# Performance work log

Measured on AMD Instinct MI355X. Metric: run time of the kernel, lower is better.

Reference implementation:

```python
import jax, jax.numpy as jnp
import numpy as np

H, D, VD = 8, 64, 64
QD, KD, VDIM, OUT = 512, 512, 512, 512
N, QS, VS = 16, 512, 512
TEMP = 10.0              # softstair_temp
SCALING = D ** -0.5


def _softstair(x):
    fl = jnp.floor(x)
    return fl + jax.nn.sigmoid(TEMP * (jnp.abs(x - fl) - 0.5))


def setup_inputs() -> dict:
    key = jax.random.key(0)
    ks = jax.random.split(key, 24)
    f = jax.random.normal
    s = 0.03  # xavier-ish scale
    return {
        "Q": f(ks[0], (N, QS, QD), jnp.float32),
        "K": f(ks[1], (N, VS, KD), jnp.float32),
        "V": f(ks[2], (N, VS, VDIM), jnp.float32),
        "past_state": f(ks[3], (N, H, QS, D), jnp.float32),
        "past_attention": jax.random.uniform(ks[4], (N, H, QS, 1), jnp.float32),
        "value_positions": jnp.arange(VS, dtype=jnp.float32),
        "attention_mask": jnp.ones((N, QS, VS), jnp.int32),
        "Wq": f(ks[5], (QD, H * D), jnp.float32) * s,
        "Wk": f(ks[6], (KD, H * D), jnp.float32) * s,
        "Wv": f(ks[7], (VDIM, H * VD), jnp.float32) * s,
        "Wpos": f(ks[8], (QD, H * D), jnp.float32) * s,
        "bpos": f(ks[9], (H * D,), jnp.float32) * s,
        "Wsigma": f(ks[10], (H, D, 1), jnp.float32) * s,
        "Wrho": f(ks[11], (H, D, 3), jnp.float32) * s,
        "mix_w": f(ks[12], (QD, 1), jnp.float32) * s,
        "mix_b": f(ks[13], (1,), jnp.float32) * s,
        "gru_wi": f(ks[14], (D, 3 * D), jnp.float32) * s,
        "gru_wh": f(ks[15], (D, 3 * D), jnp.float32) * s,
        "gru_bi": f(ks[16], (3 * D,), jnp.float32) * s,
        "gru_bh": f(ks[17], (3 * D,), jnp.float32) * s,
        "Wc": f(ks[18], (H * VD, OUT), jnp.float32) * s,
    }


def reference(Q, K, V, past_state, past_attention, value_positions, attention_mask,
              Wq, Wk, Wv, Wpos, bpos, Wsigma, Wrho, mix_w, mix_b,
              gru_wi, gru_wh, gru_bi, gru_bh, Wc):
    n, qS, _ = Q.shape
    vS = K.shape[1]
    mask_f = attention_mask.astype(jnp.float32)          # [N,qS,vS]
    mask_b = attention_mask.astype(bool)[:, None]        # [N,1,qS,vS]
    lengths = jnp.sum(mask_f, axis=-1)                   # [N,qS]
    l_1 = jnp.maximum(1.0, lengths - 1.0)[:, None, :, None]
    step_size = 1.0 / l_1                                # [N,1,qS,1]
    nvp = value_positions[None, None, None, :] * step_size  # [N,1,qS,vS]

    # mix gate
    mix = jax.nn.sigmoid(Q @ mix_w + mix_b)[:, None]     # [N,1,qS,1]

    # projections -> [N,H,S,d]
    Qpos = (Q @ Wpos + bpos).reshape(n, qS, H, D).transpose(0, 2, 1, 3)
    Qh = (Q @ Wq).reshape(n, qS, H, D).transpose(0, 2, 1, 3)
    Kh = (K @ Wk).reshape(n, vS, H, D).transpose(0, 2, 1, 3)
    Vh = (V @ Wv).reshape(n, vS, H, VD).transpose(0, 2, 1, 3)

    # content attention
    content = jnp.einsum('bhqd,bhkd->bhqk', Qh, Kh) * SCALING
    content_attn = jax.nn.softmax(jnp.where(mask_b, content, -jnp.inf), axis=-1)

    # GRUCell update (torch gate order r,z,n) on relu(Qpos) with past_state
    x = jax.nn.relu(Qpos)
    gi = x @ gru_wi + gru_bi
    gh = past_state @ gru_wh + gru_bh
    ir, iz, inn = jnp.split(gi, 3, axis=-1)
    hr, hz, hn = jnp.split(gh, 3, axis=-1)
    r = jax.nn.sigmoid(ir + hr)
    z = jax.nn.sigmoid(iz + hz)
    nn_ = jnp.tanh(inn + r * hn)
    state = (1.0 - z) * nn_ + z * past_state             # [N,H,qS,D]

    # location (Gaussian) attention
    sigma = (jax.nn.relu(jnp.einsum('bhqd,hde->bhqe', state, Wsigma)) + 0.27) \
            / lengths[:, None, :, None]                  # [N,H,qS,1]
    rho = jnp.einsum('bhqd,hde->bhqe', state, Wrho)      # [N,H,qS,3]
    steps = _softstair(rho[..., 0:1])
    attn_gate = jax.nn.sigmoid(rho[..., 1:2])
    bias_gate = jax.nn.sigmoid(rho[..., 2:3])
    mu_ = steps * step_size + attn_gate * past_attention + bias_gate
    # leaky clamp to [0,1]
    mu = jnp.maximum(0.01 * mu_, jnp.minimum(mu_, 1.0 + 0.01 * mu_))
    diff = nvp - mu                                      # [N,H,qS,vS]
    gauss = jnp.exp(-(diff * diff) / (2.0 * sigma * sigma))
    g = gauss * mask_f[:, None]
    pos_attn = g / jnp.sum(g + 1e-20, axis=-1, keepdims=True)

    scores = mix * pos_attn + (1.0 - mix) * content_attn
    attended = jnp.einsum('bhqk,bhkv->bhqv', scores, Vh)
    out = attended.transpose(0, 2, 1, 3).reshape(n, qS, H * VD) @ Wc
    return out
```

## Files before the change

### kernel.cpp

```cpp
#include <hip/hip_runtime.h>


typedef __bf16 bf16;
typedef __bf16 bfx8 __attribute__((ext_vector_type(8)));
typedef float v4f __attribute__((ext_vector_type(4)));

__device__ inline float sigm(float x) { return 1.0f / (1.0f + __expf(-x)); }
__device__ inline float tanh_fast(float x) { return 1.0f - 2.0f / (__expf(2.0f * x) + 1.0f); }

__device__ inline v4f mfma16(bfx8 a, bfx8 b, v4f c) {
    return __builtin_amdgcn_mfma_f32_16x16x32_bf16(a, b, c, 0, 0, 0);
}

__device__ inline void split8(const float* __restrict__ p, bfx8& hi, bfx8& lo) {
    float4 x = *(const float4*)p;
    float4 y = *(const float4*)(p + 4);
    float v[8] = {x.x, x.y, x.z, x.w, y.x, y.y, y.z, y.w};
#pragma unroll
    for (int j = 0; j < 8; ++j) {
        bf16 h = (bf16)v[j];
        hi[j] = h;
        lo[j] = (bf16)(v[j] - (float)h);
    }
}

__device__ inline bfx8 cvt8(const float* __restrict__ p) {
    float4 x = *(const float4*)p;
    float4 y = *(const float4*)(p + 4);
    bfx8 o;
    o[0] = (bf16)x.x; o[1] = (bf16)x.y; o[2] = (bf16)x.z; o[3] = (bf16)x.w;
    o[4] = (bf16)y.x; o[5] = (bf16)y.y; o[6] = (bf16)y.z; o[7] = (bf16)y.w;
    return o;
}

struct TW { const float* src[5]; bf16* dst[5]; bf16* dstlo[5]; };

__global__ __launch_bounds__(256) void trans_w_kernel(TW a) {
    __shared__ float tile[64][68];
    const float* src = a.src[blockIdx.y];
    bf16* dst = a.dst[blockIdx.y];
    bf16* dlo = a.dstlo[blockIdx.y];
    const int rbase = (blockIdx.x >> 3) * 64, cbase = (blockIdx.x & 7) * 64;
    const int t = threadIdx.x;
    const int r = t >> 2, cc = (t & 3) * 16;
    {
        const float* p = src + (long)(rbase + r) * 512 + cbase + cc;
        *(float4*)(&tile[r][cc]) = *(const float4*)p;
        *(float4*)(&tile[r][cc + 4]) = *(const float4*)(p + 4);
        *(float4*)(&tile[r][cc + 8]) = *(const float4*)(p + 8);
        *(float4*)(&tile[r][cc + 12]) = *(const float4*)(p + 12);
    }
    __syncthreads();
    {
        bfx8 h0, h1, l0, l1;
#pragma unroll
        for (int j = 0; j < 8; ++j) {
            float v0 = tile[cc + j][r];
            float v1 = tile[cc + 8 + j][r];
            bf16 a0 = (bf16)v0, a1 = (bf16)v1;
            h0[j] = a0; l0[j] = (bf16)(v0 - (float)a0);
            h1[j] = a1; l1[j] = (bf16)(v1 - (float)a1);
        }
        bf16* p = dst + (long)(cbase + r) * 512 + rbase + cc;
        *(bfx8*)p = h0;
        *(bfx8*)(p + 8) = h1;
        if (dlo) {
            bf16* pl = dlo + (long)(cbase + r) * 512 + rbase + cc;
            *(bfx8*)pl = l0;
            *(bfx8*)(pl + 8) = l1;
        }
    }
}

__global__ void gru_prep_kernel(const float* __restrict__ gwi, const float* __restrict__ gwh,
                                bf16* ih, bf16* il, bf16* hh, bf16* hl) {
    const float* src = blockIdx.x ? gwh : gwi;
    bf16* dh = blockIdx.x ? hh : ih;
    bf16* dl = blockIdx.x ? hl : il;
    int n = threadIdx.x;
    for (int k = 0; k < 64; ++k) {
        float v = src[k * 192 + n];
        bf16 h = (bf16)v;
        dh[n * 64 + k] = h;
        dl[n * 64 + k] = (bf16)(v - (float)h);
    }
}

struct G3 { const float* A[3]; const bf16* BT[3]; bf16* C[3]; };

__global__ __launch_bounds__(256) void gemm_bt3(G3 g) {
    __shared__ bf16 As[64][72];
    __shared__ bf16 Bs[64][72];

    const int z = blockIdx.z;
    const float* __restrict__ A = g.A[z];
    const bf16* __restrict__ BT = g.BT[z];
    bf16* __restrict__ C = g.C[z];

    const int mbase = blockIdx.x * 64, nbase = blockIdx.y * 64;
    const int t = threadIdx.x;
    const int wave = t >> 6, lane = t & 63;
    const int quad = lane >> 4, c = lane & 15;
    const int wrow = (wave >> 1) * 32, wcol = (wave & 1) * 32;

    const v4f zero4 = {0.f, 0.f, 0.f, 0.f};
    v4f acc[2][2];
    acc[0][0] = zero4; acc[0][1] = zero4; acc[1][0] = zero4; acc[1][1] = zero4;

    const int sr = t >> 2, sch = t & 3;

    for (int k0 = 0; k0 < 512; k0 += 32) {
        bfx8 va = cvt8(A + (long)(mbase + sr) * 512 + k0 + sch * 8);
        bfx8 vb = *(const bfx8*)(BT + (long)(nbase + sr) * 512 + k0 + sch * 8);
        *(bfx8*)(&As[sr][sch * 8]) = va;
        *(bfx8*)(&Bs[sr][sch * 8]) = vb;
        __syncthreads();

        bfx8 a0 = *(const bfx8*)(&As[wrow + c][quad * 8]);
        bfx8 a1 = *(const bfx8*)(&As[wrow + 16 + c][quad * 8]);
        bfx8 b0 = *(const bfx8*)(&Bs[wcol + c][quad * 8]);
        bfx8 b1 = *(const bfx8*)(&Bs[wcol + 16 + c][quad * 8]);
        acc[0][0] = mfma16(a0, b0, acc[0][0]);
        acc[0][1] = mfma16(a0, b1, acc[0][1]);
        acc[1][0] = mfma16(a1, b0, acc[1][0]);
        acc[1][1] = mfma16(a1, b1, acc[1][1]);
        __syncthreads();
    }

    if (z == 2) {
#pragma unroll
        for (int tm = 0; tm < 2; ++tm)
#pragma unroll
            for (int tn = 0; tn < 2; ++tn)
#pragma unroll
                for (int i = 0; i < 4; ++i) {
                    int rl = wrow + tm * 16 + quad * 4 + i;
                    int cl = wcol + tn * 16 + c;
                    As[cl][rl] = (bf16)acc[tm][tn][i];
                }
        __syncthreads();
        bf16* CT = C + ((long)(mbase >> 9)) * 262144 + (long)nbase * 512 + (mbase & 511);
        const int rr = t >> 2, kc = (t & 3) * 16;
        bfx8 o0, o1;
#pragma unroll
        for (int j = 0; j < 8; ++j) { o0[j] = As[rr][kc + j]; o1[j] = As[rr][kc + 8 + j]; }
        *(bfx8*)(CT + (long)rr * 512 + kc) = o0;
        *(bfx8*)(CT + (long)rr * 512 + kc + 8) = o1;
    } else {
#pragma unroll
        for (int tm = 0; tm < 2; ++tm)
#pragma unroll
            for (int tn = 0; tn < 2; ++tn)
#pragma unroll
                for (int i = 0; i < 4; ++i) {
                    int row = mbase + wrow + tm * 16 + quad * 4 + i;
                    int col = nbase + wcol + tn * 16 + c;
                    C[(long)row * 512 + col] = (bf16)acc[tm][tn][i];
                }
    }
}

__global__ __launch_bounds__(256) void gemm_out(
    const bf16* __restrict__ A, const bf16* __restrict__ BT, float* __restrict__ C) {
    __shared__ bf16 As[64][72];
    __shared__ bf16 Bs[64][72];

    const int mbase = blockIdx.x * 64, nbase = blockIdx.y * 64;
    const int t = threadIdx.x;
    const int wave = t >> 6, lane = t & 63;
    const int quad = lane >> 4, c = lane & 15;
    const int wrow = (wave >> 1) * 32, wcol = (wave & 1) * 32;

    const v4f zero4 = {0.f, 0.f, 0.f, 0.f};
    v4f acc[2][2];
    acc[0][0] = zero4; acc[0][1] = zero4; acc[1][0] = zero4; acc[1][1] = zero4;

    const int sr = t >> 2, sch = t & 3;

    for (int k0 = 0; k0 < 512; k0 += 32) {
        bfx8 va = *(const bfx8*)(A + (long)(mbase + sr) * 512 + k0 + sch * 8);
        bfx8 vb = *(const bfx8*)(BT + (long)(nbase + sr) * 512 + k0 + sch * 8);
        *(bfx8*)(&As[sr][sch * 8]) = va;
        *(bfx8*)(&Bs[sr][sch * 8]) = vb;
        __syncthreads();

        bfx8 a0 = *(const bfx8*)(&As[wrow + c][quad * 8]);
        bfx8 a1 = *(const bfx8*)(&As[wrow + 16 + c][quad * 8]);
        bfx8 b0 = *(const bfx8*)(&Bs[wcol + c][quad * 8]);
        bfx8 b1 = *(const bfx8*)(&Bs[wcol + 16 + c][quad * 8]);
        acc[0][0] = mfma16(a0, b0, acc[0][0]);
        acc[0][1] = mfma16(a0, b1, acc[0][1]);
        acc[1][0] = mfma16(a1, b0, acc[1][0]);
        acc[1][1] = mfma16(a1, b1, acc[1][1]);
        __syncthreads();
    }

#pragma unroll
    for (int tm = 0; tm < 2; ++tm)
#pragma unroll
        for (int tn = 0; tn < 2; ++tn)
#pragma unroll
            for (int i = 0; i < 4; ++i) {
                int row = mbase + wrow + tm * 16 + quad * 4 + i;
                int col = nbase + wcol + tn * 16 + c;
                C[(long)row * 512 + col] = acc[tm][tn][i];
            }
}

__global__ __launch_bounds__(256) void gemm_split_hl(
    const float* __restrict__ A, const bf16* __restrict__ BTh,
    const bf16* __restrict__ BTl, const float* __restrict__ bias,
    bf16* __restrict__ Ch, bf16* __restrict__ Cl) {
    __shared__ bf16 Ah[64][72], Al[64][72];
    __shared__ bf16 Bh[64][72], Bl[64][72];

    const int mbase = blockIdx.x * 64, nbase = blockIdx.y * 64;
    const int t = threadIdx.x;
    const int wave = t >> 6, lane = t & 63;
    const int quad = lane >> 4, c = lane & 15;
    const int wrow = (wave >> 1) * 32, wcol = (wave & 1) * 32;

    const v4f zero4 = {0.f, 0.f, 0.f, 0.f};
    v4f acc[2][2];
    acc[0][0] = zero4; acc[0][1] = zero4; acc[1][0] = zero4; acc[1][1] = zero4;

    const int sr = t >> 2, sch = t & 3;

    for (int k0 = 0; k0 < 512; k0 += 32) {
        bfx8 h, l;
        split8(A + (long)(mbase + sr) * 512 + k0 + sch * 8, h, l);
        *(bfx8*)(&Ah[sr][sch * 8]) = h;
        *(bfx8*)(&Al[sr][sch * 8]) = l;
        *(bfx8*)(&Bh[sr][sch * 8]) = *(const bfx8*)(BTh + (long)(nbase + sr) * 512 + k0 + sch * 8);
        *(bfx8*)(&Bl[sr][sch * 8]) = *(const bfx8*)(BTl + (long)(nbase + sr) * 512 + k0 + sch * 8);
        __syncthreads();

        bfx8 ah0 = *(const bfx8*)(&Ah[wrow + c][quad * 8]);
        bfx8 ah1 = *(const bfx8*)(&Ah[wrow + 16 + c][quad * 8]);
        bfx8 al0 = *(const bfx8*)(&Al[wrow + c][quad * 8]);
        bfx8 al1 = *(const bfx8*)(&Al[wrow + 16 + c][quad * 8]);
        bfx8 bh0 = *(const bfx8*)(&Bh[wcol + c][quad * 8]);
        bfx8 bh1 = *(const bfx8*)(&Bh[wcol + 16 + c][quad * 8]);
        bfx8 bl0 = *(const bfx8*)(&Bl[wcol + c][quad * 8]);
        bfx8 bl1 = *(const bfx8*)(&Bl[wcol + 16 + c][quad * 8]);
        acc[0][0] = mfma16(ah0, bh0, acc[0][0]);
        acc[0][0] = mfma16(ah0, bl0, acc[0][0]);
        acc[0][0] = mfma16(al0, bh0, acc[0][0]);
        acc[0][1] = mfma16(ah0, bh1, acc[0][1]);
        acc[0][1] = mfma16(ah0, bl1, acc[0][1]);
        acc[0][1] = mfma16(al0, bh1, acc[0][1]);
        acc[1][0] = mfma16(ah1, bh0, acc[1][0]);
        acc[1][0] = mfma16(ah1, bl0, acc[1][0]);
        acc[1][0] = mfma16(al1, bh0, acc[1][0]);
        acc[1][1] = mfma16(ah1, bh1, acc[1][1]);
        acc[1][1] = mfma16(ah1, bl1, acc[1][1]);
        acc[1][1] = mfma16(al1, bh1, acc[1][1]);
        __syncthreads();
    }

#pragma unroll
    for (int tm = 0; tm < 2; ++tm)
#pragma unroll
        for (int tn = 0; tn < 2; ++tn)
#pragma unroll
            for (int i = 0; i < 4; ++i) {
                int row = mbase + wrow + tm * 16 + quad * 4 + i;
                int col = nbase + wcol + tn * 16 + c;
                float v = fmaxf(acc[tm][tn][i] + bias[col], 0.f);
                bf16 h = (bf16)v;
                Ch[(long)row * 512 + col] = h;
                Cl[(long)row * 512 + col] = (bf16)(v - (float)h);
            }
}

__global__ __launch_bounds__(256) void mix_len_kernel(
    const float* __restrict__ Q, const int* __restrict__ mask,
    const float* __restrict__ mix_w, const float* __restrict__ mix_b,
    float* __restrict__ mixv, float* __restrict__ stepv, float* __restrict__ lenv,
    unsigned* __restrict__ maskbits) {
    int row = blockIdx.x * 4 + (threadIdx.x >> 6);
    int lane = threadIdx.x & 63;
    float dot = 0.f, ms = 0.f;
    unsigned myw = 0;
#pragma unroll
    for (int j = 0; j < 8; ++j) {
        float qv = Q[(long)row * 512 + j * 64 + lane];
        float wv = mix_w[j * 64 + lane];
        dot += qv * wv;
        int mv = mask[(long)row * 512 + j * 64 + lane];
        unsigned long long b = __ballot(mv != 0);
        ms += (float)__popcll(b);
        if ((lane >> 1) == j) myw = (unsigned)(b >> ((lane & 1) * 32));
    }
#pragma unroll
    for (int o = 32; o > 0; o >>= 1) dot += __shfl_xor(dot, o);
    if (lane < 16) maskbits[(long)row * 16 + lane] = myw;
    if (lane == 0) {
        mixv[row] = sigm(dot + mix_b[0]);
        lenv[row] = ms;
        stepv[row] = 1.0f / fmaxf(1.0f, ms - 1.0f);
    }
}

__global__ __launch_bounds__(256) void gru_fused_kernel(
    const bf16* __restrict__ Xh, const bf16* __restrict__ Xl,
    const float* __restrict__ hp,
    const bf16* __restrict__ wih, const bf16* __restrict__ wil,
    const bf16* __restrict__ whh, const bf16* __restrict__ whl,
    const float* __restrict__ gbi, const float* __restrict__ gbh,
    const float* __restrict__ pa, const float* __restrict__ Wsigma,
    const float* __restrict__ Wrho,
    const float* __restrict__ lenv, const float* __restrict__ stepv,
    float* __restrict__ muv, float* __restrict__ sigv) {
    __shared__ bf16 Wh[192][72], Wl[192][72];
    __shared__ float biL[384];

    const int b = blockIdx.x;
    const int qb = b & 7, nh = b >> 3, hd = nh & 7, n = nh >> 3;
    const int t = threadIdx.x;
    const int w = t >> 6, lane = t & 63, quad = lane >> 4, c = lane & 15;
    const int q0 = qb * 64 + w * 16;

    if (t < 192) { biL[t] = gbi[t]; biL[192 + t] = gbh[t]; }
#pragma unroll
    for (int it = 0; it < 6; ++it) {
        int task = it * 256 + t;
        int r = task >> 3, ch = task & 7;
        *(bfx8*)(&Wh[r][ch * 8]) = *(const bfx8*)(wih + r * 64 + ch * 8);
        *(bfx8*)(&Wl[r][ch * 8]) = *(const bfx8*)(wil + r * 64 + ch * 8);
    }
    __syncthreads();

    const v4f zero4 = {0.f, 0.f, 0.f, 0.f};
    v4f gi[12], gh[12];
#pragma unroll
    for (int nt = 0; nt < 12; ++nt) gi[nt] = zero4;
#pragma unroll
    for (int ks = 0; ks < 2; ++ks) {
        long ao = (long)(n * 512 + q0 + c) * 512 + hd * 64 + ks * 32 + quad * 8;
        bfx8 xh = *(const bfx8*)(Xh + ao);
        bfx8 xl = *(const bfx8*)(Xl + ao);
#pragma unroll
        for (int nt = 0; nt < 12; ++nt) {
            bfx8 bh = *(const bfx8*)(&Wh[nt * 16 + c][ks * 32 + quad * 8]);
            bfx8 bl = *(const bfx8*)(&Wl[nt * 16 + c][ks * 32 + quad * 8]);
            gi[nt] = mfma16(xh, bh, gi[nt]);
            gi[nt] = mfma16(xh, bl, gi[nt]);
            gi[nt] = mfma16(xl, bh, gi[nt]);
        }
    }
    __syncthreads();
#pragma unroll
    for (int it = 0; it < 6; ++it) {
        int task = it * 256 + t;
        int r = task >> 3, ch = task & 7;
        *(bfx8*)(&Wh[r][ch * 8]) = *(const bfx8*)(whh + r * 64 + ch * 8);
        *(bfx8*)(&Wl[r][ch * 8]) = *(const bfx8*)(whl + r * 64 + ch * 8);
    }
    __syncthreads();
#pragma unroll
    for (int nt = 0; nt < 12; ++nt) gh[nt] = zero4;
#pragma unroll
    for (int ks = 0; ks < 2; ++ks) {
        bfx8 ah, al;
        split8(hp + (long)(nh * 512 + q0 + c) * 64 + ks * 32 + quad * 8, ah, al);
#pragma unroll
        for (int nt = 0; nt < 12; ++nt) {
            bfx8 bh = *(const bfx8*)(&Wh[nt * 16 + c][ks * 32 + quad * 8]);
            bfx8 bl = *(const bfx8*)(&Wl[nt * 16 + c][ks * 32 + quad * 8]);
            gh[nt] = mfma16(ah, bh, gh[nt]);
            gh[nt] = mfma16(ah, bl, gh[nt]);
            gh[nt] = mfma16(al, bh, gh[nt]);
        }
    }

    float st[4][4];
#pragma unroll
    for (int t4 = 0; t4 < 4; ++t4) {
        float bir = biL[t4 * 16 + c];
        float biz = biL[64 + t4 * 16 + c];
        float bin = biL[128 + t4 * 16 + c];
        float bhr = biL[192 + t4 * 16 + c];
        float bhz = biL[256 + t4 * 16 + c];
        float bhn = biL[320 + t4 * 16 + c];
#pragma unroll
        for (int i = 0; i < 4; ++i) {
            int row = q0 + quad * 4 + i;
            float r = sigm(gi[t4][i] + bir + gh[t4][i] + bhr);
            float z = sigm(gi[t4 + 4][i] + biz + gh[t4 + 4][i] + bhz);
            float nn_ = tanh_fast(gi[t4 + 8][i] + bin + r * (gh[t4 + 8][i] + bhn));
            float hpv = hp[(long)(nh * 512 + row) * 64 + t4 * 16 + c];
            st[t4][i] = (1.0f - z) * nn_ + z * hpv;
        }
    }

    float ws_[4], wr0[4], wr1[4], wr2[4];
#pragma unroll
    for (int t4 = 0; t4 < 4; ++t4) {
        int d = t4 * 16 + c;
        ws_[t4] = Wsigma[hd * 64 + d];
        wr0[t4] = Wrho[(hd * 64 + d) * 3 + 0];
        wr1[t4] = Wrho[(hd * 64 + d) * 3 + 1];
        wr2[t4] = Wrho[(hd * 64 + d) * 3 + 2];
    }
#pragma unroll
    for (int i = 0; i < 4; ++i) {
        float s0 = 0.f, s1 = 0.f, s2 = 0.f, s3 = 0.f;
#pragma unroll
        for (int t4 = 0; t4 < 4; ++t4) {
            float sv = st[t4][i];
            s0 += sv * ws_[t4];
            s1 += sv * wr0[t4];
            s2 += sv * wr1[t4];
            s3 += sv * wr2[t4];
        }
#pragma unroll
        for (int o = 1; o < 16; o <<= 1) {
            s0 += __shfl_xor(s0, o);
            s1 += __shfl_xor(s1, o);
            s2 += __shfl_xor(s2, o);
            s3 += __shfl_xor(s3, o);
        }
        if (c == 0) {
            int row = q0 + quad * 4 + i;
            int idx = nh * 512 + row, rq = n * 512 + row;
            float L = lenv[rq], sp = stepv[rq];
            float sg = (fmaxf(s0, 0.f) + 0.27f) / L;
            float fl = floorf(s1);
            float steps = fl + sigm(10.0f * (fabsf(s1 - fl) - 0.5f));
            float ag = sigm(s2), bg = sigm(s3);
            float mu_ = steps * sp + ag * pa[idx] + bg;
            float mu = fmaxf(0.01f * mu_, fminf(mu_, 1.0f + 0.01f * mu_));
            muv[idx] = mu;
            sigv[idx] = sg;
        }
    }
}

__global__ __launch_bounds__(256) void attn_fused_kernel(
    const bf16* __restrict__ Qh, const bf16* __restrict__ Kh,
    const bf16* __restrict__ VhT, const unsigned* __restrict__ maskbits,
    const float* __restrict__ vpos, const float* __restrict__ mixv,
    const float* __restrict__ stepv, const float* __restrict__ muv,
    const float* __restrict__ sigv, bf16* __restrict__ att) {
    __shared__ bf16 Pp[16][520];
    __shared__ bf16 Pg[16][520];
    __shared__ float rsum[4][16], rgsum[4][16];

    const int b = blockIdx.x;
    const int nh = ((b >> 8) << 3) | (b & 7);
    const int qt = (b >> 3) & 31;
    const int hd = nh & 7, n = nh >> 3;
    const int t = threadIdx.x;
    const int wave = t >> 6, lane = t & 63;
    const int quad = lane >> 4, c = lane & 15;
    const int qloc = quad * 4;

    const bf16* qrow = Qh + (long)(n * 512 + qt * 16 + c) * 512 + hd * 64 + quad * 8;
    bfx8 afr0 = *(const bfx8*)qrow;
    bfx8 afr1 = *(const bfx8*)(qrow + 32);

    const v4f zero4 = {0.f, 0.f, 0.f, 0.f};
    v4f acc[8];
#pragma unroll
    for (int i = 0; i < 8; ++i) acc[i] = zero4;

    const bf16* kbase = Kh + (long)(n * 512 + wave * 128 + c) * 512 + hd * 64 + quad * 8;
#pragma unroll
    for (int t8 = 0; t8 < 8; ++t8) {
        bfx8 b0 = *(const bfx8*)(kbase + (long)t8 * 16 * 512);
        bfx8 b1 = *(const bfx8*)(kbase + (long)t8 * 16 * 512 + 32);
        acc[t8] = mfma16(afr0, b0, acc[t8]);
        acc[t8] = mfma16(afr1, b1, acc[t8]);
    }

    float mu_[4], i2s[4], stp[4];
#pragma unroll
    for (int i = 0; i < 4; ++i) {
        int q = qt * 16 + qloc + i;
        int idx = nh * 512 + q, rq = n * 512 + q;
        mu_[i] = muv[idx];
        float sg = sigv[idx];
        i2s[i] = 0.5f / (sg * sg);
        stp[i] = stepv[rq];
    }

    unsigned mbits[4];
    {
        const unsigned* mrow = maskbits + ((long)(n * 512 + qt * 16) << 4) + wave * 4;
#pragma unroll
        for (int i = 0; i < 4; ++i) {
            const unsigned* mr = mrow + ((qloc + i) << 4);
            unsigned w0 = mr[0], w1 = mr[1], w2 = mr[2], w3 = mr[3];
            mbits[i] = ((w0 >> c) & 1u) | (((w0 >> (16 + c)) & 1u) << 1) |
                       (((w1 >> c) & 1u) << 2) | (((w1 >> (16 + c)) & 1u) << 3) |
                       (((w2 >> c) & 1u) << 4) | (((w2 >> (16 + c)) & 1u) << 5) |
                       (((w3 >> c) & 1u) << 6) | (((w3 >> (16 + c)) & 1u) << 7);
        }
    }

    float vp[8];
#pragma unroll
    for (int t8 = 0; t8 < 8; ++t8) vp[t8] = vpos[wave * 128 + t8 * 16 + c];

    float psum[4] = {0.f, 0.f, 0.f, 0.f};
    float gsum[4] = {0.f, 0.f, 0.f, 0.f};
#pragma unroll
    for (int i = 0; i < 4; ++i) {
        float m = mu_[i], s = stp[i], c2 = i2s[i];
#pragma unroll
        for (int t8 = 0; t8 < 8; ++t8) {
            int on = (mbits[i] >> t8) & 1;
            float pv = on ? __expf(acc[t8][i] * 0.125f) : 0.f;
            float d = vp[t8] * s - m;
            float gv = on ? __expf(-(d * d) * c2) : 0.f;
            psum[i] += pv;
            gsum[i] += gv;
            int k = wave * 128 + t8 * 16 + c;
            Pp[qloc + i][k] = (bf16)pv;
            Pg[qloc + i][k] = (bf16)gv;
        }
    }
#pragma unroll
    for (int i = 0; i < 4; ++i) {
#pragma unroll
        for (int o = 1; o < 16; o <<= 1) {
            psum[i] += __shfl_xor(psum[i], o);
            gsum[i] += __shfl_xor(gsum[i], o);
        }
        if (c == 0) {
            rsum[wave][qloc + i] = psum[i];
            rgsum[wave][qloc + i] = gsum[i];
        }
    }

    __syncthreads();

    float ac[4], bc[4];
#pragma unroll
    for (int i = 0; i < 4; ++i) {
        float Sp = rsum[0][qloc + i] + rsum[1][qloc + i] + rsum[2][qloc + i] + rsum[3][qloc + i];
        float Sg = rgsum[0][qloc + i] + rgsum[1][qloc + i] + rgsum[2][qloc + i] +
                   rgsum[3][qloc + i] + 512.0f * 1e-20f;
        float m_ = mixv[n * 512 + qt * 16 + qloc + i];
        ac[i] = (1.0f - m_) / Sp;
        bc[i] = m_ / Sg;
    }

    v4f accP = zero4, accG = zero4;
    const bf16* vrow = VhT + (long)(n * 512 + hd * 64 + wave * 16 + c) * 512 + quad * 8;
#pragma unroll
    for (int ks = 0; ks < 16; ++ks) {
        bfx8 bf_ = *(const bfx8*)(vrow + ks * 32);
        bfx8 ap = *(const bfx8*)(&Pp[c][ks * 32 + quad * 8]);
        bfx8 ag = *(const bfx8*)(&Pg[c][ks * 32 + quad * 8]);
        accP = mfma16(ap, bf_, accP);
        accG = mfma16(ag, bf_, accG);
    }

#pragma unroll
    for (int i = 0; i < 4; ++i) {
        att[(long)(n * 512 + qt * 16 + quad * 4 + i) * 512 + hd * 64 + wave * 16 + c] =
            (bf16)(ac[i] * accP[i] + bc[i] * accG[i]);
    }
}

extern "C" void kernel_launch(void* const* d_in, const int* in_sizes, int n_in,
                              void* d_out, int out_size, void* d_ws, size_t ws_size,
                              hipStream_t stream) {
    (void)in_sizes; (void)n_in; (void)out_size; (void)ws_size;

    const float* Q = (const float*)d_in[0];
    const float* K = (const float*)d_in[1];
    const float* V = (const float*)d_in[2];
    const float* past_state = (const float*)d_in[3];
    const float* past_att = (const float*)d_in[4];
    const float* vpos = (const float*)d_in[5];
    const int* mask = (const int*)d_in[6];
    const float* Wq = (const float*)d_in[7];
    const float* Wk = (const float*)d_in[8];
    const float* Wv = (const float*)d_in[9];
    const float* Wpos = (const float*)d_in[10];
    const float* bpos = (const float*)d_in[11];
    const float* Wsigma = (const float*)d_in[12];
    const float* Wrho = (const float*)d_in[13];
    const float* mix_w = (const float*)d_in[14];
    const float* mix_b = (const float*)d_in[15];
    const float* gwi = (const float*)d_in[16];
    const float* gwh = (const float*)d_in[17];
    const float* gbi = (const float*)d_in[18];
    const float* gbh = (const float*)d_in[19];
    const float* Wc = (const float*)d_in[20];
    float* out = (float*)d_out;

    char* p = (char*)d_ws;
    const size_t SZB = 8192UL * 512 * 2;
    const size_t SZW = 512UL * 512 * 2;
    bf16* WqT = (bf16*)p;   p += SZW;
    bf16* WkT = (bf16*)p;   p += SZW;
    bf16* WvT = (bf16*)p;   p += SZW;
    bf16* WpT = (bf16*)p;   p += SZW;
    bf16* WpTl = (bf16*)p;  p += SZW;
    bf16* WcT = (bf16*)p;   p += SZW;
    bf16* wih = (bf16*)p;   p += 24576;
    bf16* wil = (bf16*)p;   p += 24576;
    bf16* whh = (bf16*)p;   p += 24576;
    bf16* whl = (bf16*)p;   p += 24576;
    bf16* Qh = (bf16*)p;    p += SZB;
    bf16* Kh = (bf16*)p;    p += SZB;
    bf16* VhT = (bf16*)p;   p += SZB;
    bf16* Xh = (bf16*)p;
    bf16* att = Xh;         p += SZB;
    bf16* Xl = (bf16*)p;    p += SZB;
    unsigned* maskbits = (unsigned*)p;   p += 8192UL * 16 * 4;
    float* mixv = (float*)p;  p += 32768;
    float* stepv = (float*)p; p += 32768;
    float* lenv = (float*)p;  p += 32768;
    float* muv = (float*)p;   p += 262144;
    float* sigv = (float*)p;  p += 262144;

    dim3 blk(256);
    dim3 gProj(128, 8, 1);

    TW tw;
    tw.src[0] = Wq; tw.src[1] = Wk; tw.src[2] = Wv; tw.src[3] = Wpos; tw.src[4] = Wc;
    tw.dst[0] = WqT; tw.dst[1] = WkT; tw.dst[2] = WvT; tw.dst[3] = WpT; tw.dst[4] = WcT;
    tw.dstlo[0] = nullptr; tw.dstlo[1] = nullptr; tw.dstlo[2] = nullptr;
    tw.dstlo[3] = WpTl; tw.dstlo[4] = nullptr;
    trans_w_kernel<<<dim3(64, 5), blk, 0, stream>>>(tw);

    gru_prep_kernel<<<dim3(2), dim3(192), 0, stream>>>(gwi, gwh, wih, wil, whh, whl);

    G3 g;
    g.A[0] = Q; g.A[1] = K; g.A[2] = V;
    g.BT[0] = WqT; g.BT[1] = WkT; g.BT[2] = WvT;
    g.C[0] = Qh; g.C[1] = Kh; g.C[2] = VhT;
    gemm_bt3<<<dim3(128, 8, 3), blk, 0, stream>>>(g);

    gemm_split_hl<<<gProj, blk, 0, stream>>>(Q, WpT, WpTl, bpos, Xh, Xl);

    mix_len_kernel<<<dim3(2048), blk, 0, stream>>>(Q, mask, mix_w, mix_b, mixv, stepv, lenv, maskbits);

    gru_fused_kernel<<<dim3(1024), blk, 0, stream>>>(
        Xh, Xl, past_state, wih, wil, whh, whl, gbi, gbh, past_att, Wsigma, Wrho,
        lenv, stepv, muv, sigv);

    attn_fused_kernel<<<dim3(4096), blk, 0, stream>>>(
        Qh, Kh, VhT, maskbits, vpos, mixv, stepv, muv, sigv, att);

    gemm_out<<<gProj, blk, 0, stream>>>(att, WcT, out);
}
```

Measured before the change: 347.4 us.

## Unify projection GEMMs into 128x128-tile kernel with async LDS loads and XOR swizzle

Replaces the separate 64x64 projection GEMMs (Q/K/V, split hi/lo positional, and output) with one 128x128-tile kernel. It uses direct global-to-LDS loads for bf16 operands and XOR-swizzled LDS and global layouts for the weights and attention output, so the loads go straight into a conflict-free shared layout. The split-precision positional projection now runs as three sequential k-phases instead of three MFMAs per step, and all four input projections go out in one launch. The cost is a larger per-thread register tile (16 accumulators), fewer blocks per launch, and a swizzled storage convention that every producer and consumer must match.

```diff
diff --git a/kernel.cpp b/kernel.cpp
--- a/kernel.cpp
+++ b/kernel.cpp
@@ -10,6 +10,13 @@
 
 __device__ inline v4f mfma16(bfx8 a, bfx8 b, v4f c) {
     return __builtin_amdgcn_mfma_f32_16x16x32_bf16(a, b, c, 0, 0, 0);
+}
+
+typedef const __attribute__((address_space(1))) void* gvp;
+typedef __attribute__((address_space(3))) void* lvp;
+
+__device__ inline void gload_lds16(const bf16* g, bf16* l) {
+    __builtin_amdgcn_global_load_lds((gvp)g, (lvp)l, 16, 0, 0);
 }
 
 __device__ inline void split8(const float* __restrict__ p, bfx8& hi, bfx8& lo) {
@@ -22,15 +29,6 @@
         hi[j] = h;
         lo[j] = (bf16)(v[j] - (float)h);
     }
-}
-
-__device__ inline bfx8 cvt8(const float* __restrict__ p) {
-    float4 x = *(const float4*)p;
-    float4 y = *(const float4*)(p + 4);
-    bfx8 o;
-    o[0] = (bf16)x.x; o[1] = (bf16)x.y; o[2] = (bf16)x.z; o[3] = (bf16)x.w;
-    o[4] = (bf16)y.x; o[5] = (bf16)y.y; o[6] = (bf16)y.z; o[7] = (bf16)y.w;
-    return o;
 }
 
 struct TW { const float* src[5]; bf16* dst[5]; bf16* dstlo[5]; };
@@ -61,13 +59,16 @@
             h0[j] = a0; l0[j] = (bf16)(v0 - (float)a0);
             h1[j] = a1; l1[j] = (bf16)(v1 - (float)a1);
         }
-        bf16* p = dst + (long)(cbase + r) * 512 + rbase + cc;
-        *(bfx8*)p = h0;
-        *(bfx8*)(p + 8) = h1;
+        const int n_ = cbase + r;
+        const int x_ = (n_ & 7) << 3;
+        const long rowo = (long)n_ * 512;
+        const int ka = (rbase + cc) ^ x_;
+        const int kb = (rbase + cc + 8) ^ x_;
+        *(bfx8*)(dst + rowo + ka) = h0;
+        *(bfx8*)(dst + rowo + kb) = h1;
         if (dlo) {
-            bf16* pl = dlo + (long)(cbase + r) * 512 + rbase + cc;
-            *(bfx8*)pl = l0;
-            *(bfx8*)(pl + 8) = l1;
+            *(bfx8*)(dlo + rowo + ka) = l0;
+            *(bfx8*)(dlo + rowo + kb) = l1;
         }
     }
 }
@@ -86,191 +87,189 @@
     }
 }
 
-struct G3 { const float* A[3]; const bf16* BT[3]; bf16* C[3]; };
-
-__global__ __launch_bounds__(256) void gemm_bt3(G3 g) {
-    __shared__ bf16 As[64][72];
-    __shared__ bf16 Bs[64][72];
-
-    const int z = blockIdx.z;
-    const float* __restrict__ A = g.A[z];
-    const bf16* __restrict__ BT = g.BT[z];
-    bf16* __restrict__ C = g.C[z];
-
-    const int mbase = blockIdx.x * 64, nbase = blockIdx.y * 64;
-    const int t = threadIdx.x;
-    const int wave = t >> 6, lane = t & 63;
-    const int quad = lane >> 4, c = lane & 15;
-    const int wrow = (wave >> 1) * 32, wcol = (wave & 1) * 32;
+struct GEMMDesc {
+    const float* Af;
+    const bf16* Ab;
+    const bf16* B0;
+    const bf16* B1;
+    const float* bias;
+    bf16* Cb;
+    bf16* Cl;
+    float* Cf;
+    int mode;
+};
+struct G4 { GEMMDesc d[4]; };
+
+__global__ __launch_bounds__(256, 4) void gemm128(G4 gg) {
+    __shared__ bf16 sm[16384];
+    bf16* As = sm;
+    bf16* Bs = sm + 8192;
+
+    const GEMMDesc g = gg.d[blockIdx.z];
+    const int mode = g.mode;
+    const int mbase = blockIdx.x * 128, nbase = blockIdx.y * 128;
+    const int t = threadIdx.x, w = t >> 6, l = t & 63;
+    const int quad = l >> 4, c = l & 15;
+    const int wr = w >> 1, wc = w & 1;
 
     const v4f zero4 = {0.f, 0.f, 0.f, 0.f};
-    v4f acc[2][2];
-    acc[0][0] = zero4; acc[0][1] = zero4; acc[1][0] = zero4; acc[1][1] = zero4;
-
-    const int sr = t >> 2, sch = t & 3;
-
-    for (int k0 = 0; k0 < 512; k0 += 32) {
-        bfx8 va = cvt8(A + (long)(mbase + sr) * 512 + k0 + sch * 8);
-        bfx8 vb = *(const bfx8*)(BT + (long)(nbase + sr) * 512 + k0 + sch * 8);
-        *(bfx8*)(&As[sr][sch * 8]) = va;
-        *(bfx8*)(&Bs[sr][sch * 8]) = vb;
+    v4f acc[4][4];
+#pragma unroll
+    for (int m = 0; m < 4; ++m)
+#pragma unroll
+        for (int nn = 0; nn < 4; ++nn) acc[m][nn] = zero4;
+
+    const int nsteps = (mode == 2) ? 24 : 8;
+    const int arow_t = t >> 3;
+    const int ach = t & 7;
+    const int asw = ((ach ^ (arow_t & 7)) * 8);
+    const int xm = c & 7;
+
+    for (int s = 0; s < nsteps; ++s) {
+        const bf16* Bsrc = g.B0;
+        int k0;
+        bool lo = false;
+        if (mode == 2) {
+            int ph = s >> 3;
+            k0 = (s & 7) * 64;
+            if (ph == 1) Bsrc = g.B1;
+            lo = (ph == 2);
+        } else {
+            k0 = s * 64;
+        }
+
+#pragma unroll
+        for (int j = 0; j < 4; ++j) {
+            int slot = w * 4 + j;
+            int row = slot * 8 + (l >> 3);
+            const bf16* src = Bsrc + (long)(nbase + row) * 512 + k0 + (l & 7) * 8;
+            gload_lds16(src, Bs + slot * 512);
+        }
+        if (mode == 3) {
+#pragma unroll
+            for (int j = 0; j < 4; ++j) {
+                int slot = w * 4 + j;
+                int row = slot * 8 + (l >> 3);
+                const bf16* src = g.Ab + (long)(mbase + row) * 512 + k0 + (l & 7) * 8;
+                gload_lds16(src, As + slot * 512);
+            }
+        } else {
+#pragma unroll
+            for (int j = 0; j < 4; ++j) {
+                int row = j * 32 + arow_t;
+                const float* p = g.Af + (long)(mbase + row) * 512 + k0 + ach * 8;
+                float4 x = *(const float4*)p, y = *(const float4*)(p + 4);
+                float v[8] = {x.x, x.y, x.z, x.w, y.x, y.y, y.z, y.w};
+                bfx8 hv;
+                if (!lo) {
+#pragma unroll
+                    for (int q = 0; q < 8; ++q) hv[q] = (bf16)v[q];
+                } else {
+#pragma unroll
+                    for (int q = 0; q < 8; ++q) {
+                        bf16 h = (bf16)v[q];
+                        hv[q] = (bf16)(v[q] - (float)h);
+                    }
+                }
+                *(bfx8*)(&As[row * 64 + asw]) = hv;
+            }
+        }
         __syncthreads();
 
-        bfx8 a0 = *(const bfx8*)(&As[wrow + c][quad * 8]);
-        bfx8 a1 = *(const bfx8*)(&As[wrow + 16 + c][quad * 8]);
-        bfx8 b0 = *(const bfx8*)(&Bs[wcol + c][quad * 8]);
-        bfx8 b1 = *(const bfx8*)(&Bs[wcol + 16 + c][quad * 8]);
-        acc[0][0] = mfma16(a0, b0, acc[0][0]);
-        acc[0][1] = mfma16(a0, b1, acc[0][1]);
-        acc[1][0] = mfma16(a1, b0, acc[1][0]);
-        acc[1][1] = mfma16(a1, b1, acc[1][1]);
+#pragma unroll
+        for (int ks = 0; ks < 2; ++ks) {
+            const int off = (((ks * 4 + quad) ^ xm) * 8);
+            bfx8 af[4], bb[4];
+#pragma unroll
+            for (int m = 0; m < 4; ++m)
+                af[m] = *(const bfx8*)(&As[(wr * 64 + m * 16 + c) * 64 + off]);
+#pragma unroll
+            for (int nn = 0; nn < 4; ++nn)
+                bb[nn] = *(const bfx8*)(&Bs[(wc * 64 + nn * 16 + c) * 64 + off]);
+#pragma unroll
+            for (int m = 0; m < 4; ++m)
+#pragma unroll
+                for (int nn = 0; nn < 4; ++nn)
+                    acc[m][nn] = mfma16(af[m], bb[nn], acc[m][nn]);
+        }
         __syncthreads();
     }
 
-    if (z == 2) {
-#pragma unroll
-        for (int tm = 0; tm < 2; ++tm)
-#pragma unroll
-            for (int tn = 0; tn < 2; ++tn)
+    if (mode == 3) {
+        float* C = g.Cf;
+#pragma unroll
+        for (int m = 0; m < 4; ++m)
+#pragma unroll
+            for (int nn = 0; nn < 4; ++nn)
 #pragma unroll
                 for (int i = 0; i < 4; ++i) {
-                    int rl = wrow + tm * 16 + quad * 4 + i;
-                    int cl = wcol + tn * 16 + c;
-                    As[cl][rl] = (bf16)acc[tm][tn][i];
+                    int row = mbase + wr * 64 + m * 16 + quad * 4 + i;
+                    int col = nbase + wc * 64 + nn * 16 + c;
+                    C[(long)row * 512 + col] = acc[m][nn][i];
                 }
+        return;
+    }
+
+    if (mode == 1) {
+        bf16* CT = g.Cb + ((long)(mbase >> 9)) * 262144;
+        const int s0 = mbase & 511;
+        for (int h = 0; h < 2; ++h) {
+            if (wr == h) {
+#pragma unroll
+                for (int m = 0; m < 4; ++m)
+#pragma unroll
+                    for (int nn = 0; nn < 4; ++nn)
+#pragma unroll
+                        for (int i = 0; i < 4; ++i)
+                            sm[(wc * 64 + nn * 16 + c) * 64 + m * 16 + quad * 4 + i] =
+                                (bf16)acc[m][nn][i];
+            }
+            __syncthreads();
+            {
+                const bf16* src = sm + (t >> 1) * 64 + (t & 1) * 32;
+                bf16* d = CT + (long)(nbase + (t >> 1)) * 512 + s0 + h * 64 + (t & 1) * 32;
+#pragma unroll
+                for (int j = 0; j < 4; ++j) *(bfx8*)(d + j * 8) = *(const bfx8*)(src + j * 8);
+            }
+            __syncthreads();
+        }
+        return;
+    }
+
+    for (int h = 0; h < 2; ++h) {
+        if (wr == h) {
+#pragma unroll
+            for (int m = 0; m < 4; ++m)
+#pragma unroll
+                for (int nn = 0; nn < 4; ++nn)
+#pragma unroll
+                    for (int i = 0; i < 4; ++i) {
+                        int col = wc * 64 + nn * 16 + c;
+                        float v = acc[m][nn][i];
+                        if (mode == 2) v = fmaxf(v + g.bias[nbase + col], 0.f);
+                        bf16 hv = (bf16)v;
+                        sm[(m * 16 + quad * 4 + i) * 128 + col] = hv;
+                        if (mode == 2)
+                            sm[8192 + (m * 16 + quad * 4 + i) * 128 + col] =
+                                (bf16)(v - (float)hv);
+                    }
+        }
         __syncthreads();
-        bf16* CT = C + ((long)(mbase >> 9)) * 262144 + (long)nbase * 512 + (mbase & 511);
-        const int rr = t >> 2, kc = (t & 3) * 16;
-        bfx8 o0, o1;
-#pragma unroll
-        for (int j = 0; j < 8; ++j) { o0[j] = As[rr][kc + j]; o1[j] = As[rr][kc + 8 + j]; }
-        *(bfx8*)(CT + (long)rr * 512 + kc) = o0;
-        *(bfx8*)(CT + (long)rr * 512 + kc + 8) = o1;
-    } else {
-#pragma unroll
-        for (int tm = 0; tm < 2; ++tm)
-#pragma unroll
-            for (int tn = 0; tn < 2; ++tn)
-#pragma unroll
-                for (int i = 0; i < 4; ++i) {
-                    int row = mbase + wrow + tm * 16 + quad * 4 + i;
-                    int col = nbase + wcol + tn * 16 + c;
-                    C[(long)row * 512 + col] = (bf16)acc[tm][tn][i];
-                }
-    }
-}
-
-__global__ __launch_bounds__(256) void gemm_out(
-    const bf16* __restrict__ A, const bf16* __restrict__ BT, float* __restrict__ C) {
-    __shared__ bf16 As[64][72];
-    __shared__ bf16 Bs[64][72];
-
-    const int mbase = blockIdx.x * 64, nbase = blockIdx.y * 64;
-    const int t = threadIdx.x;
-    const int wave = t >> 6, lane = t & 63;
-    const int quad = lane >> 4, c = lane & 15;
-    const int wrow = (wave >> 1) * 32, wcol = (wave & 1) * 32;
-
-    const v4f zero4 = {0.f, 0.f, 0.f, 0.f};
-    v4f acc[2][2];
-    acc[0][0] = zero4; acc[0][1] = zero4; acc[1][0] = zero4; acc[1][1] = zero4;
-
-    const int sr = t >> 2, sch = t & 3;
-
-    for (int k0 = 0; k0 < 512; k0 += 32) {
-        bfx8 va = *(const bfx8*)(A + (long)(mbase + sr) * 512 + k0 + sch * 8);
-        bfx8 vb = *(const bfx8*)(BT + (long)(nbase + sr) * 512 + k0 + sch * 8);
-        *(bfx8*)(&As[sr][sch * 8]) = va;
-        *(bfx8*)(&Bs[sr][sch * 8]) = vb;
+        {
+            const int row = t >> 2, seg = t & 3;
+            const bf16* src = sm + row * 128 + seg * 32;
+            bf16* d = g.Cb + (long)(mbase + h * 64 + row) * 512 + nbase + seg * 32;
+#pragma unroll
+            for (int j = 0; j < 4; ++j) *(bfx8*)(d + j * 8) = *(const bfx8*)(src + j * 8);
+            if (mode == 2) {
+                const bf16* src2 = sm + 8192 + row * 128 + seg * 32;
+                bf16* d2 = g.Cl + (long)(mbase + h * 64 + row) * 512 + nbase + seg * 32;
+#pragma unroll
+                for (int j = 0; j < 4; ++j) *(bfx8*)(d2 + j * 8) = *(const bfx8*)(src2 + j * 8);
+            }
+        }
         __syncthreads();
-
-        bfx8 a0 = *(const bfx8*)(&As[wrow + c][quad * 8]);
-        bfx8 a1 = *(const bfx8*)(&As[wrow + 16 + c][quad * 8]);
-        bfx8 b0 = *(const bfx8*)(&Bs[wcol + c][quad * 8]);
-        bfx8 b1 = *(const bfx8*)(&Bs[wcol + 16 + c][quad * 8]);
-        acc[0][0] = mfma16(a0, b0, acc[0][0]);
-        acc[0][1] = mfma16(a0, b1, acc[0][1]);
-        acc[1][0] = mfma16(a1, b0, acc[1][0]);
-        acc[1][1] = mfma16(a1, b1, acc[1][1]);
-        __syncthreads();
-    }
-
-#pragma unroll
-    for (int tm = 0; tm < 2; ++tm)
-#pragma unroll
-        for (int tn = 0; tn < 2; ++tn)
-#pragma unroll
-            for (int i = 0; i < 4; ++i) {
-                int row = mbase + wrow + tm * 16 + quad * 4 + i;
-                int col = nbase + wcol + tn * 16 + c;
-                C[(long)row * 512 + col] = acc[tm][tn][i];
-            }
-}
-
-__global__ __launch_bounds__(256) void gemm_split_hl(
-    const float* __restrict__ A, const bf16* __restrict__ BTh,
-    const bf16* __restrict__ BTl, const float* __restrict__ bias,
-    bf16* __restrict__ Ch, bf16* __restrict__ Cl) {
-    __shared__ bf16 Ah[64][72], Al[64][72];
-    __shared__ bf16 Bh[64][72], Bl[64][72];
-
-    const int mbase = blockIdx.x * 64, nbase = blockIdx.y * 64;
-    const int t = threadIdx.x;
-    const int wave = t >> 6, lane = t & 63;
-    const int quad = lane >> 4, c = lane & 15;
-    const int wrow = (wave >> 1) * 32, wcol = (wave & 1) * 32;
-
-    const v4f zero4 = {0.f, 0.f, 0.f, 0.f};
-    v4f acc[2][2];
-    acc[0][0] = zero4; acc[0][1] = zero4; acc[1][0] = zero4; acc[1][1] = zero4;
-
-    const int sr = t >> 2, sch = t & 3;
-
-    for (int k0 = 0; k0 < 512; k0 += 32) {
-        bfx8 h, l;
-        split8(A + (long)(mbase + sr) * 512 + k0 + sch * 8, h, l);
-        *(bfx8*)(&Ah[sr][sch * 8]) = h;
-        *(bfx8*)(&Al[sr][sch * 8]) = l;
-        *(bfx8*)(&Bh[sr][sch * 8]) = *(const bfx8*)(BTh + (long)(nbase + sr) * 512 + k0 + sch * 8);
-        *(bfx8*)(&Bl[sr][sch * 8]) = *(const bfx8*)(BTl + (long)(nbase + sr) * 512 + k0 + sch * 8);
-        __syncthreads();
-
-        bfx8 ah0 = *(const bfx8*)(&Ah[wrow + c][quad * 8]);
-        bfx8 ah1 = *(const bfx8*)(&Ah[wrow + 16 + c][quad * 8]);
-        bfx8 al0 = *(const bfx8*)(&Al[wrow + c][quad * 8]);
-        bfx8 al1 = *(const bfx8*)(&Al[wrow + 16 + c][quad * 8]);
-        bfx8 bh0 = *(const bfx8*)(&Bh[wcol + c][quad * 8]);
-        bfx8 bh1 = *(const bfx8*)(&Bh[wcol + 16 + c][quad * 8]);
-        bfx8 bl0 = *(const bfx8*)(&Bl[wcol + c][quad * 8]);
-        bfx8 bl1 = *(const bfx8*)(&Bl[wcol + 16 + c][quad * 8]);
-        acc[0][0] = mfma16(ah0, bh0, acc[0][0]);
-        acc[0][0] = mfma16(ah0, bl0, acc[0][0]);
-        acc[0][0] = mfma16(al0, bh0, acc[0][0]);
-        acc[0][1] = mfma16(ah0, bh1, acc[0][1]);
-        acc[0][1] = mfma16(ah0, bl1, acc[0][1]);
-        acc[0][1] = mfma16(al0, bh1, acc[0][1]);
-        acc[1][0] = mfma16(ah1, bh0, acc[1][0]);
-        acc[1][0] = mfma16(ah1, bl0, acc[1][0]);
-        acc[1][0] = mfma16(al1, bh0, acc[1][0]);
-        acc[1][1] = mfma16(ah1, bh1, acc[1][1]);
-        acc[1][1] = mfma16(ah1, bl1, acc[1][1]);
-        acc[1][1] = mfma16(al1, bh1, acc[1][1]);
-        __syncthreads();
-    }
-
-#pragma unroll
-    for (int tm = 0; tm < 2; ++tm)
-#pragma unroll
-        for (int tn = 0; tn < 2; ++tn)
-#pragma unroll
-            for (int i = 0; i < 4; ++i) {
-                int row = mbase + wrow + tm * 16 + quad * 4 + i;
-                int col = nbase + wcol + tn * 16 + c;
-                float v = fmaxf(acc[tm][tn][i] + bias[col], 0.f);
-                bf16 h = (bf16)v;
-                Ch[(long)row * 512 + col] = h;
-                Cl[(long)row * 512 + col] = (bf16)(v - (float)h);
-            }
+    }
 }
 
 __global__ __launch_bounds__(256) void mix_len_kernel(
@@ -560,7 +559,9 @@
 
 #pragma unroll
     for (int i = 0; i < 4; ++i) {
-        att[(long)(n * 512 + qt * 16 + quad * 4 + i) * 512 + hd * 64 + wave * 16 + c] =
+        int q = qt * 16 + quad * 4 + i;
+        int cx = (wave * 16 + c) ^ (((quad * 4 + i) & 7) << 3);
+        att[(long)(n * 512 + q) * 512 + hd * 64 + cx] =
             (bf16)(ac[i] * accP[i] + bc[i] * accG[i]);
     }
 }
@@ -620,7 +621,6 @@
     float* sigv = (float*)p;  p += 262144;
 
     dim3 blk(256);
-    dim3 gProj(128, 8, 1);
 
     TW tw;
     tw.src[0] = Wq; tw.src[1] = Wk; tw.src[2] = Wv; tw.src[3] = Wpos; tw.src[4] = Wc;
@@ -631,15 +631,18 @@
 
     gru_prep_kernel<<<dim3(2), dim3(192), 0, stream>>>(gwi, gwh, wih, wil, whh, whl);
 
-    G3 g;
-    g.A[0] = Q; g.A[1] = K; g.A[2] = V;
-    g.BT[0] = WqT; g.BT[1] = WkT; g.BT[2] = WvT;
-    g.C[0] = Qh; g.C[1] = Kh; g.C[2] = VhT;
-    gemm_bt3<<<dim3(128, 8, 3), blk, 0, stream>>>(g);
-
-    gemm_split_hl<<<gProj, blk, 0, stream>>>(Q, WpT, WpTl, bpos, Xh, Xl);
-
     mix_len_kernel<<<dim3(2048), blk, 0, stream>>>(Q, mask, mix_w, mix_b, mixv, stepv, lenv, maskbits);
+
+    G4 gp;
+    gp.d[0].Af = Q;  gp.d[0].Ab = nullptr; gp.d[0].B0 = WpT; gp.d[0].B1 = WpTl;
+    gp.d[0].bias = bpos; gp.d[0].Cb = Xh; gp.d[0].Cl = Xl; gp.d[0].Cf = nullptr; gp.d[0].mode = 2;
+    gp.d[1].Af = Q;  gp.d[1].Ab = nullptr; gp.d[1].B0 = WqT; gp.d[1].B1 = nullptr;
+    gp.d[1].bias = nullptr; gp.d[1].Cb = Qh; gp.d[1].Cl = nullptr; gp.d[1].Cf = nullptr; gp.d[1].mode = 0;
+    gp.d[2].Af = K;  gp.d[2].Ab = nullptr; gp.d[2].B0 = WkT; gp.d[2].B1 = nullptr;
+    gp.d[2].bias = nullptr; gp.d[2].Cb = Kh; gp.d[2].Cl = nullptr; gp.d[2].Cf = nullptr; gp.d[2].mode = 0;
+    gp.d[3].Af = V;  gp.d[3].Ab = nullptr; gp.d[3].B0 = WvT; gp.d[3].B1 = nullptr;
+    gp.d[3].bias = nullptr; gp.d[3].Cb = VhT; gp.d[3].Cl = nullptr; gp.d[3].Cf = nullptr; gp.d[3].mode = 1;
+    gemm128<<<dim3(64, 4, 4), blk, 0, stream>>>(gp);
 
     gru_fused_kernel<<<dim3(1024), blk, 0, stream>>>(
         Xh, Xl, past_state, wih, wil, whh, whl, gbi, gbh, past_att, Wsigma, Wrho,
@@ -648,5 +651,10 @@
     attn_fused_kernel<<<dim3(4096), blk, 0, stream>>>(
         Qh, Kh, VhT, maskbits, vpos, mixv, stepv, muv, sigv, att);
 
-    gemm_out<<<gProj, blk, 0, stream>>>(att, WcT, out);
-}
+    G4 go;
+    go.d[0].Af = nullptr; go.d[0].Ab = att; go.d[0].B0 = WcT; go.d[0].B1 = nullptr;
+    go.d[0].bias = nullptr; go.d[0].Cb = nullptr; go.d[0].Cl = nullptr; go.d[0].Cf = out;
+    go.d[0].mode = 3;
+    go.d[1] = go.d[0]; go.d[2] = go.d[0]; go.d[3] = go.d[0];
+    gemm128<<<dim3(64, 4, 1), blk, 0, stream>>>(go);
+}
```

Measured after the change: 370.7 us. 6.7% more time.
